# Performance work log

Measured on AMD Instinct MI355X. Metric: run time of the kernel, lower is better.

Reference implementation:

```python
import jax, jax.numpy as jnp
import numpy as np

B, T, C, SIZE = 2, 4096, 1024, 1024
ROPE_DIM = 64
GAMMA = 0.96


def setup_inputs() -> dict:
    key = jax.random.key(0)
    ks = jax.random.split(key, 8)
    x = jax.random.normal(ks[0], (B, T, C), dtype=jnp.float32)
    group_mask = jax.random.randint(ks[1], (B, T), 0, 2).astype(jnp.float32)
    att_mask = jnp.ones((B, T), dtype=jnp.float32)
    # torch init: randn(in, out) / in
    W_Q = jax.random.normal(ks[2], (C, SIZE), dtype=jnp.float32) / C
    W_K = jax.random.normal(ks[3], (C, SIZE), dtype=jnp.float32) / C
    W_V = jax.random.normal(ks[4], (C, SIZE), dtype=jnp.float32) / C
    fc_w = jax.random.normal(ks[5], (SIZE, SIZE), dtype=jnp.float32) / np.float32(np.sqrt(SIZE))
    fc_b = jnp.zeros((SIZE,), dtype=jnp.float32)
    return dict(x=x, group_mask=group_mask, att_mask=att_mask,
                W_Q=W_Q, W_K=W_K, W_V=W_V, fc_w=fc_w, fc_b=fc_b)


def _rope(t, offset):
    # lucidrains rotate_queries_or_keys: rotate first ROPE_DIM features of
    # the last dim, interleaved-pair rotation, positions along axis -2.
    seq = t.shape[-2]
    inv = 1.0 / (10000.0 ** (jnp.arange(0, ROPE_DIM, 2, dtype=jnp.float32) / ROPE_DIM))
    pos = jnp.arange(seq, dtype=jnp.float32) + offset
    freqs = pos[:, None] * inv[None, :]              # [T, D/2]
    freqs = jnp.repeat(freqs, 2, axis=-1)            # [T, D]
    cos, sin = jnp.cos(freqs), jnp.sin(freqs)
    t_rot, t_pass = t[..., :ROPE_DIM], t[..., ROPE_DIM:]
    x1, x2 = t_rot[..., 0::2], t_rot[..., 1::2]
    rot_half = jnp.stack([-x2, x1], axis=-1).reshape(t_rot.shape)
    t_rot = t_rot * cos + rot_half * sin
    return jnp.concatenate([t_rot, t_pass], axis=-1)


def reference(x, group_mask, att_mask, W_Q, W_K, W_V, fc_w, fc_b):
    Bx, Tx, _ = x.shape
    # _qkv with apply_rope=True, apply_act=True (ReLU)
    Q = jax.nn.relu(_rope(x @ W_Q, 0))               # [B,T,SIZE]
    K = jax.nn.relu(_rope(x @ W_K, 0))
    V = jax.nn.relu(x @ W_V)
    n = jnp.arange(Tx)[:, None]
    m = jnp.arange(Tx)[None, :]
    causal = (n >= m)
    # decay mask D[n,m] = gamma^(n-m) for n>=m else 0
    D = jnp.where(causal, jnp.float32(GAMMA) ** (n - m).astype(jnp.float32), 0.0)
    # group mask G[b,n,m] = group_mask[b, n-m] for n>=m else 0
    idx = jnp.clip(n - m, 0, Tx - 1)                 # [T,T]
    G = group_mask[:, idx] * causal.astype(x.dtype)  # [B,T,T]
    A = jnp.einsum('bnd,bmd->bnm', Q, K)
    A = A * att_mask[:, :, None]                     # attention mask
    A = A * D[None, :, :]                            # decay mask
    A = A * G                                        # group mask
    y = jnp.einsum('bnm,bmd->bnd', A, V)
    y = y @ fc_w + fc_b
    return y
```

## Files before the change

kernel.cpp:

```cpp
#include <hip/hip_runtime.h>
#include <stdint.h>

typedef __attribute__((ext_vector_type(4))) float f32x4;
typedef __attribute__((ext_vector_type(8))) __bf16 bf16x8;
typedef __attribute__((ext_vector_type(4))) unsigned short u16x4;
typedef __attribute__((ext_vector_type(8))) unsigned short u16x8;

#define DEV __device__ __forceinline__

DEV unsigned short f2bf(float f) {
  union { float f; unsigned int u; } v; v.f = f;
  unsigned int r = v.u + 0x7fffu + ((v.u >> 16) & 1u);
  return (unsigned short)(r >> 16);
}

DEV void gl_lds16(const void* g, void* l) {
  __builtin_amdgcn_global_load_lds(
      (const __attribute__((address_space(1))) unsigned int*)g,
      (__attribute__((address_space(3))) unsigned int*)l, 16, 0, 0);
}


__global__ void prep_rope(float* __restrict__ costab, float* __restrict__ sintab) {
  int idx = blockIdx.x * 256 + threadIdx.x;
  int n = idx >> 6, c = idx & 63, j = c >> 1;
  float inv = powf(10000.0f, -(float)(2 * j) / 64.0f);
  float ang = (float)n * inv;
  costab[idx] = cosf(ang);
  sintab[idx] = sinf(ang);
}

__global__ void prep_wtab(const float* __restrict__ gm, float* __restrict__ wtab) {
  int t = threadIdx.x;
  int b = t >> 9, d = t & 511;
  wtab[t] = gm[b * 4096 + d] * powf(0.96f, (float)d);
}

__global__ void cvt_x(const float* __restrict__ x, unsigned short* __restrict__ xb) {
  size_t i8 = ((size_t)blockIdx.x * 256 + threadIdx.x) * 8;
  float4 a = *(const float4*)(x + i8);
  float4 b = *(const float4*)(x + i8 + 4);
  u16x8 o;
  o[0] = f2bf(a.x); o[1] = f2bf(a.y); o[2] = f2bf(a.z); o[3] = f2bf(a.w);
  o[4] = f2bf(b.x); o[5] = f2bf(b.y); o[6] = f2bf(b.z); o[7] = f2bf(b.w);
  *(u16x8*)(xb + i8) = o;
}

__global__ void transpose_cvt(const float* __restrict__ src, unsigned short* __restrict__ dst) {
  __shared__ float tile[32][33];
  int tx = threadIdx.x & 31, ty = threadIdx.x >> 5;
  int c0 = blockIdx.x * 32, r0 = blockIdx.y * 32;
  #pragma unroll
  for (int j = 0; j < 4; j++)
    tile[ty + 8 * j][tx] = src[(size_t)(r0 + ty + 8 * j) * 1024 + c0 + tx];
  __syncthreads();
  #pragma unroll
  for (int j = 0; j < 4; j++)
    dst[(size_t)(c0 + ty + 8 * j) * 1024 + r0 + tx] = f2bf(tile[tx][ty + 8 * j]);
}

template<int EPI>
__global__ void __launch_bounds__(256, 2)
gemm128(const unsigned short* __restrict__ A,
        const unsigned short* __restrict__ Bt,
        unsigned short* __restrict__ q_out,
        unsigned short* __restrict__ k_out,
        unsigned short* __restrict__ vt_out,
        const float* __restrict__ costab,
        const float* __restrict__ sintab,
        float* __restrict__ f_out,
        const float* __restrict__ bias)
{
  constexpr int K = 1024;
  __shared__ char smem[32768];
  char* a_sm = smem;
  char* b_sm = smem + 16384;
  const int tid = threadIdx.x;
  const int lane = tid & 63;
  const int w = tid >> 6;
  const int wm = w >> 1, wn = w & 1;
  const int bm = blockIdx.x, bn = blockIdx.y;

  const f32x4 fz = {0.f, 0.f, 0.f, 0.f};
  f32x4 acc[4][4];
  #pragma unroll
  for (int i = 0; i < 4; i++)
    #pragma unroll
    for (int j = 0; j < 4; j++) acc[i][j] = fz;

  const unsigned short* Abase = A + (size_t)bm * 128 * K;
  const unsigned short* Bbase = Bt + (size_t)bn * 128 * K;

  for (int k0 = 0; k0 < K; k0 += 64) {
    __syncthreads();
    #pragma unroll
    for (int i = 0; i < 4; i++) {
      int tg = i * 256 + tid;
      int row = tg >> 3;
      int sl = (tg & 7) ^ (row & 7);
      gl_lds16(Abase + (size_t)row * K + k0 + sl * 8, a_sm + tg * 16);
    }
    #pragma unroll
    for (int i = 0; i < 4; i++) {
      int tg = i * 256 + tid;
      int row = tg >> 3;
      int sl = (tg & 7) ^ (row & 7);
      gl_lds16(Bbase + (size_t)row * K + k0 + sl * 8, b_sm + tg * 16);
    }
    __syncthreads();
    #pragma unroll
    for (int ks = 0; ks < 2; ks++) {
      int kb = ks * 64 + ((lane >> 4) << 4);
      bf16x8 af[4], bfv[4];
      #pragma unroll
      for (int f = 0; f < 4; f++) {
        int ar = wm * 64 + f * 16 + (lane & 15);
        af[f] = *(const bf16x8*)(a_sm + ar * 128 + (kb ^ ((ar & 7) << 4)));
        int br = wn * 64 + f * 16 + (lane & 15);
        bfv[f] = *(const bf16x8*)(b_sm + br * 128 + (kb ^ ((br & 7) << 4)));
      }
      #pragma unroll
      for (int fm = 0; fm < 4; fm++)
        #pragma unroll
        for (int fn = 0; fn < 4; fn++)
          acc[fm][fn] = __builtin_amdgcn_mfma_f32_16x16x32_bf16(af[fm], bfv[fn], acc[fm][fn], 0, 0, 0);
    }
  }

  const int rbase = bm * 128 + wm * 64 + ((lane >> 4) << 2);
  const int cbase = bn * 128 + wn * 64;

  if constexpr (EPI == 0) {
    #pragma unroll
    for (int fn = 0; fn < 4; fn++) {
      int col = cbase + fn * 16 + (lane & 15);
      int which = col >> 10;
      int c = col & 1023;
      #pragma unroll
      for (int fm = 0; fm < 4; fm++) {
        int row0 = rbase + fm * 16;
        float vals[4];
        #pragma unroll
        for (int r = 0; r < 4; r++) vals[r] = acc[fm][fn][r];
        if (which < 2) {
          if (c < 64) {
            #pragma unroll
            for (int r = 0; r < 4; r++) {
              float p = __shfl_xor(vals[r], 1);
              int n = (row0 + r) & 4095;
              float cs = costab[n * 64 + c];
              float sn = sintab[n * 64 + c];
              float rh = (c & 1) ? p : -p;
              vals[r] = vals[r] * cs + rh * sn;
            }
          }
          unsigned short* dst = (which == 0) ? q_out : k_out;
          #pragma unroll
          for (int r = 0; r < 4; r++) {
            float v = vals[r] > 0.f ? vals[r] : 0.f;
            dst[(size_t)(row0 + r) * 1024 + c] = f2bf(v);
          }
        } else {
          u16x4 sv;
          #pragma unroll
          for (int r = 0; r < 4; r++) {
            float v = vals[r] > 0.f ? vals[r] : 0.f;
            sv[r] = f2bf(v);
          }
          *(u16x4*)(vt_out + (size_t)c * 8192 + row0) = sv;
        }
      }
    }
  } else {
    #pragma unroll
    for (int fn = 0; fn < 4; fn++) {
      int col = cbase + fn * 16 + (lane & 15);
      float bv = bias[col];
      #pragma unroll
      for (int fm = 0; fm < 4; fm++) {
        int row0 = rbase + fm * 16;
        #pragma unroll
        for (int r = 0; r < 4; r++)
          f_out[(size_t)(row0 + r) * 1024 + col] = acc[fm][fn][r] + bv;
      }
    }
  }
}

__global__ void __launch_bounds__(512, 2)
attn_kernel(const unsigned short* __restrict__ Qb,
            const unsigned short* __restrict__ Kb,
            const unsigned short* __restrict__ Vt,
            const float* __restrict__ wtab,
            const float* __restrict__ att_mask,
            unsigned short* __restrict__ Yb)
{
  __shared__ char smem[49152];
  __shared__ float wl[320];
  char* k_sm = smem;
  char* q_sm = smem + 40960;
  char* p_sm = smem;

  const int tid = threadIdx.x;
  const int lane = tid & 63;
  const int w = tid >> 6;
  const int q0 = blockIdx.x * 64;
  const int b = blockIdx.y;
  const int base = b * 4096;
  const int kv0 = q0 - 256;

  if (tid < 320) wl[tid] = wtab[b * 512 + tid];

  const int wq = w >> 2, wk = w & 3;
  const f32x4 fz = {0.f, 0.f, 0.f, 0.f};
  f32x4 sacc[2][5];
  #pragma unroll
  for (int i = 0; i < 2; i++)
    #pragma unroll
    for (int j = 0; j < 5; j++) sacc[i][j] = fz;

  for (int c0 = 0; c0 < 1024; c0 += 64) {
    __syncthreads();
    {
      int row = tid >> 3;
      int sl = (tid & 7) ^ (row & 7);
      gl_lds16(Qb + (size_t)(base + q0 + row) * 1024 + c0 + sl * 8, q_sm + tid * 16);
    }
    #pragma unroll
    for (int i = 0; i < 5; i++) {
      int tg = i * 512 + tid;
      int row = tg >> 3;
      int sl = (tg & 7) ^ (row & 7);
      int m = kv0 + row; m = m < 0 ? 0 : m;
      gl_lds16(Kb + (size_t)(base + m) * 1024 + c0 + sl * 8, k_sm + tg * 16);
    }
    __syncthreads();
    #pragma unroll
    for (int ks = 0; ks < 2; ks++) {
      int kb = ks * 64 + ((lane >> 4) << 4);
      bf16x8 af[2], bfv[5];
      #pragma unroll
      for (int f = 0; f < 2; f++) {
        int ar = wq * 32 + f * 16 + (lane & 15);
        af[f] = *(const bf16x8*)(q_sm + ar * 128 + (kb ^ ((ar & 7) << 4)));
      }
      #pragma unroll
      for (int f = 0; f < 5; f++) {
        int br = wk * 80 + f * 16 + (lane & 15);
        bfv[f] = *(const bf16x8*)(k_sm + br * 128 + (kb ^ ((br & 7) << 4)));
      }
      #pragma unroll
      for (int fm = 0; fm < 2; fm++)
        #pragma unroll
        for (int fj = 0; fj < 5; fj++)
          sacc[fm][fj] = __builtin_amdgcn_mfma_f32_16x16x32_bf16(af[fm], bfv[fj], sacc[fm][fj], 0, 0, 0);
    }
  }
  __syncthreads();

  #pragma unroll
  for (int fm = 0; fm < 2; fm++) {
    #pragma unroll
    for (int fj = 0; fj < 5; fj++) {
      int jj = wk * 80 + fj * 16 + (lane & 15);
      int m = kv0 + jj;
      #pragma unroll
      for (int r = 0; r < 4; r++) {
        int i = wq * 32 + fm * 16 + ((lane >> 4) << 2) + r;
        int d = 256 + i - jj;
        float wgt = (d >= 0 && m >= 0) ? wl[d] : 0.f;
        *(unsigned short*)(p_sm + i * 640 + ((jj * 2) ^ ((i & 7) << 4))) =
            f2bf(sacc[fm][fj][r] * wgt);
      }
    }
  }
  __syncthreads();

  f32x4 yacc[4][8];
  #pragma unroll
  for (int i = 0; i < 4; i++)
    #pragma unroll
    for (int j = 0; j < 8; j++) yacc[i][j] = fz;

  for (int kt = 0; kt < 10; kt++) {
    int kb = kt * 64 + ((lane >> 4) << 4);
    bf16x8 pa[4], vb[8];
    #pragma unroll
    for (int f = 0; f < 4; f++) {
      int i = f * 16 + (lane & 15);
      pa[f] = *(const bf16x8*)(p_sm + i * 640 + (kb ^ ((i & 7) << 4)));
    }
    int kvi = kt * 32 + ((lane >> 4) << 3);
    int m = kv0 + kvi; m = m < 0 ? 0 : m;
    #pragma unroll
    for (int f = 0; f < 8; f++) {
      int col = w * 128 + f * 16 + (lane & 15);
      vb[f] = *(const bf16x8*)(Vt + (size_t)col * 8192 + base + m);
    }
    #pragma unroll
    for (int fm = 0; fm < 4; fm++)
      #pragma unroll
      for (int fn = 0; fn < 8; fn++)
        yacc[fm][fn] = __builtin_amdgcn_mfma_f32_16x16x32_bf16(pa[fm], vb[fn], yacc[fm][fn], 0, 0, 0);
  }

  #pragma unroll
  for (int fm = 0; fm < 4; fm++) {
    #pragma unroll
    for (int r = 0; r < 4; r++) {
      int n = q0 + fm * 16 + ((lane >> 4) << 2) + r;
      float am = att_mask[base + n];
      #pragma unroll
      for (int fn = 0; fn < 8; fn++) {
        int col = w * 128 + fn * 16 + (lane & 15);
        Yb[(size_t)(base + n) * 1024 + col] = f2bf(yacc[fm][fn][r] * am);
      }
    }
  }
}

extern "C" void kernel_launch(void* const* d_in, const int* in_sizes, int n_in,
                              void* d_out, int out_size, void* d_ws, size_t ws_size,
                              hipStream_t stream)
{
  (void)in_sizes; (void)n_in; (void)out_size;
  const float* x   = (const float*)d_in[0];
  const float* gm  = (const float*)d_in[1];
  const float* am  = (const float*)d_in[2];
  const float* wq  = (const float*)d_in[3];
  const float* wk  = (const float*)d_in[4];
  const float* wv  = (const float*)d_in[5];
  const float* fcw = (const float*)d_in[6];
  const float* fcb = (const float*)d_in[7];
  float* out = (float*)d_out;

  char* p = (char*)d_ws;
  unsigned short* xb    = (unsigned short*)p; p += (size_t)8192 * 1024 * 2;
  unsigned short* Qb    = (unsigned short*)p; p += (size_t)8192 * 1024 * 2;
  unsigned short* Kb    = (unsigned short*)p; p += (size_t)8192 * 1024 * 2;
  unsigned short* Vt    = (unsigned short*)p; p += (size_t)8192 * 1024 * 2;
  unsigned short* Ybuf  = (unsigned short*)p; p += (size_t)8192 * 1024 * 2;
  unsigned short* WqkvT = (unsigned short*)p; p += (size_t)3072 * 1024 * 2;
  unsigned short* FcwT  = (unsigned short*)p; p += (size_t)1024 * 1024 * 2;
  float* costab = (float*)p; p += (size_t)4096 * 64 * 4;
  float* sintab = (float*)p; p += (size_t)4096 * 64 * 4;
  float* wtab   = (float*)p; p += 4096;
  if ((size_t)(p - (char*)d_ws) > ws_size) return;

  prep_rope<<<1024, 256, 0, stream>>>(costab, sintab);
  prep_wtab<<<1, 1024, 0, stream>>>(gm, wtab);
  cvt_x<<<4096, 256, 0, stream>>>(x, xb);
  transpose_cvt<<<dim3(32, 32), 256, 0, stream>>>(wq, WqkvT);
  transpose_cvt<<<dim3(32, 32), 256, 0, stream>>>(wk, WqkvT + (size_t)1024 * 1024);
  transpose_cvt<<<dim3(32, 32), 256, 0, stream>>>(wv, WqkvT + (size_t)2048 * 1024);
  transpose_cvt<<<dim3(32, 32), 256, 0, stream>>>(fcw, FcwT);

  gemm128<0><<<dim3(64, 24), 256, 0, stream>>>(xb, WqkvT, Qb, Kb, Vt, costab, sintab, nullptr, nullptr);
  attn_kernel<<<dim3(64, 2), 512, 0, stream>>>(Qb, Kb, Vt, wtab, am, Ybuf);
  gemm128<1><<<dim3(64, 8), 256, 0, stream>>>(Ybuf, FcwT, nullptr, nullptr, nullptr, nullptr, nullptr, out, fcb);
}
```

Baseline: 244.9 us.

## Replace QKV GEMM with 256x256 pipelined tile kernel and merge prep launches

Adds a new QKV projection GEMM that uses 256x256 tiles with 512 threads and 128KB of dynamic LDS. It double-buffers half-tiles with direct global-to-LDS loads, uses explicit waitcnt, barriers and setprio to overlap loads with MFMA work, and keeps the RoPE/ReLU epilogue. The goal is higher data reuse per tile and better overlap of memory and compute. The rope and wtab prep kernels are merged into one launch, and the four weight transposes into one 3D-grid launch, to cut launch count. The trade-offs are a large LDS footprint that limits occupancy, and hand-tuned wait counts that are fragile.

```diff
diff --git a/kernel.cpp b/kernel.cpp
--- a/kernel.cpp
+++ b/kernel.cpp
@@ -20,20 +20,25 @@
       (__attribute__((address_space(3))) unsigned int*)l, 16, 0, 0);
 }
 
-
-__global__ void prep_rope(float* __restrict__ costab, float* __restrict__ sintab) {
+#define SBAR() __builtin_amdgcn_s_barrier()
+#define LGKM0() do { asm volatile("s_waitcnt lgkmcnt(0)" ::: "memory"); __builtin_amdgcn_sched_barrier(0); } while (0)
+#define VMC6() do { asm volatile("s_waitcnt vmcnt(6)" ::: "memory"); __builtin_amdgcn_sched_barrier(0); } while (0)
+#define VMC0() do { asm volatile("s_waitcnt vmcnt(0)" ::: "memory"); __builtin_amdgcn_sched_barrier(0); } while (0)
+
+
+__global__ void prep_tabs(const float* __restrict__ gm,
+                          float* __restrict__ costab, float* __restrict__ sintab,
+                          float* __restrict__ wtab) {
   int idx = blockIdx.x * 256 + threadIdx.x;
   int n = idx >> 6, c = idx & 63, j = c >> 1;
   float inv = powf(10000.0f, -(float)(2 * j) / 64.0f);
   float ang = (float)n * inv;
   costab[idx] = cosf(ang);
   sintab[idx] = sinf(ang);
-}
-
-__global__ void prep_wtab(const float* __restrict__ gm, float* __restrict__ wtab) {
-  int t = threadIdx.x;
-  int b = t >> 9, d = t & 511;
-  wtab[t] = gm[b * 4096 + d] * powf(0.96f, (float)d);
+  if (idx < 1024) {
+    int b = idx >> 9, d = idx & 511;
+    wtab[idx] = gm[b * 4096 + d] * powf(0.96f, (float)d);
+  }
 }
 
 __global__ void cvt_x(const float* __restrict__ x, unsigned short* __restrict__ xb) {
@@ -46,8 +51,13 @@
   *(u16x8*)(xb + i8) = o;
 }
 
-__global__ void transpose_cvt(const float* __restrict__ src, unsigned short* __restrict__ dst) {
+__global__ void transpose_cvt4(const float* __restrict__ s0, const float* __restrict__ s1,
+                               const float* __restrict__ s2, const float* __restrict__ s3,
+                               unsigned short* __restrict__ d0, unsigned short* __restrict__ d3) {
   __shared__ float tile[32][33];
+  int z = blockIdx.z;
+  const float* src = (z == 0) ? s0 : (z == 1) ? s1 : (z == 2) ? s2 : s3;
+  unsigned short* dst = (z == 3) ? d3 : d0 + (size_t)z * 1024 * 1024;
   int tx = threadIdx.x & 31, ty = threadIdx.x >> 5;
   int c0 = blockIdx.x * 32, r0 = blockIdx.y * 32;
   #pragma unroll
@@ -59,17 +69,189 @@
     dst[(size_t)(c0 + ty + 8 * j) * 1024 + r0 + tx] = f2bf(tile[tx][ty + 8 * j]);
 }
 
-template<int EPI>
+
+DEV void stage_half(const unsigned short* __restrict__ g0, int kcol, char* regn, int tid) {
+  #pragma unroll
+  for (int i = 0; i < 2; i++) {
+    int tg = i * 512 + tid;
+    int row = tg >> 3;
+    int ch = tg & 7;
+    gl_lds16(g0 + (size_t)row * 1024 + kcol + ((ch ^ (row & 7)) << 3), regn + tg * 16);
+  }
+}
+
+DEV void read_a4(bf16x8 (&af)[4][2], const char* regn, int wm, int lane) {
+  #pragma unroll
+  for (int f = 0; f < 4; f++) {
+    int row = wm * 64 + f * 16 + (lane & 15);
+    #pragma unroll
+    for (int ks = 0; ks < 2; ks++) {
+      int c = ks * 4 + (lane >> 4);
+      af[f][ks] = *(const bf16x8*)(regn + row * 128 + ((c ^ (row & 7)) << 4));
+    }
+  }
+}
+
+DEV void read_b2(bf16x8 (&bfr)[2][2], const char* regn, int wn, int lane) {
+  #pragma unroll
+  for (int g = 0; g < 2; g++) {
+    int row = wn * 32 + g * 16 + (lane & 15);
+    #pragma unroll
+    for (int ks = 0; ks < 2; ks++) {
+      int c = ks * 4 + (lane >> 4);
+      bfr[g][ks] = *(const bf16x8*)(regn + row * 128 + ((c ^ (row & 7)) << 4));
+    }
+  }
+}
+
+template<int MB, int NB>
+DEV void mfma16(f32x4 (&acc)[8][4], const bf16x8 (&af)[4][2], const bf16x8 (&bfr)[2][2]) {
+  #pragma unroll
+  for (int ks = 0; ks < 2; ks++)
+    #pragma unroll
+    for (int f = 0; f < 4; f++)
+      #pragma unroll
+      for (int g = 0; g < 2; g++)
+        acc[MB + f][NB + g] =
+            __builtin_amdgcn_mfma_f32_16x16x32_bf16(af[f][ks], bfr[g][ks], acc[MB + f][NB + g], 0, 0, 0);
+}
+
+__global__ void __launch_bounds__(512, 2)
+gemm256_qkv(const unsigned short* __restrict__ A,
+            const unsigned short* __restrict__ Bt,
+            unsigned short* __restrict__ q_out,
+            unsigned short* __restrict__ k_out,
+            unsigned short* __restrict__ vt_out,
+            const float* __restrict__ costab,
+            const float* __restrict__ sintab)
+{
+  extern __shared__ char smem[];
+  constexpr int K = 1024, NT = 16;
+  const int tid = threadIdx.x;
+  const int lane = tid & 63;
+  const int w = tid >> 6;
+  const int wm = w >> 2, wn = w & 3;
+  const int bm = blockIdx.x, bn = blockIdx.y;
+
+  char* rg[2][2][2];
+  #pragma unroll
+  for (int d = 0; d < 2; d++)
+    #pragma unroll
+    for (int m = 0; m < 2; m++)
+      #pragma unroll
+      for (int h = 0; h < 2; h++)
+        rg[d][m][h] = smem + d * 65536 + m * 32768 + h * 16384;
+
+  const unsigned short* Ab = A + (size_t)bm * 256 * K;
+  const unsigned short* Bb = Bt + (size_t)bn * 256 * K;
+  const unsigned short* A0g = Ab;
+  const unsigned short* A1g = Ab + (size_t)128 * K;
+  const unsigned short* B0g = Bb;
+  const unsigned short* B1g = Bb + (size_t)128 * K;
+
+  const f32x4 fz = {0.f, 0.f, 0.f, 0.f};
+  f32x4 acc[8][4];
+  #pragma unroll
+  for (int i = 0; i < 8; i++)
+    #pragma unroll
+    for (int j = 0; j < 4; j++) acc[i][j] = fz;
+
+  stage_half(A0g, 0, rg[0][0][0], tid);
+  stage_half(B0g, 0, rg[0][1][0], tid);
+  stage_half(B1g, 0, rg[0][1][1], tid);
+  stage_half(A1g, 0, rg[0][0][1], tid);
+  stage_half(A0g, 64, rg[1][0][0], tid);
+  stage_half(B1g, 64, rg[1][1][1], tid);
+  stage_half(A1g, 64, rg[1][0][1], tid);
+  VMC6();
+  SBAR();
+
+  for (int t = 0; t < NT; ++t) {
+    const int db = t & 1;
+    bf16x8 af[4][2], bfr[2][2];
+
+    read_a4(af, rg[db][0][0], wm, lane);
+    read_b2(bfr, rg[db][1][0], wn, lane);
+    if (t + 1 < NT) stage_half(B0g, (t + 1) * 64, rg[db ^ 1][1][0], tid);
+    SBAR(); LGKM0();
+    __builtin_amdgcn_s_setprio(1);
+    mfma16<0, 0>(acc, af, bfr);
+    __builtin_amdgcn_s_setprio(0);
+    SBAR();
+
+    read_b2(bfr, rg[db][1][1], wn, lane);
+    if (t + 2 < NT) stage_half(A0g, (t + 2) * 64, rg[db][0][0], tid);
+    SBAR(); LGKM0();
+    __builtin_amdgcn_s_setprio(1);
+    mfma16<0, 2>(acc, af, bfr);
+    __builtin_amdgcn_s_setprio(0);
+    SBAR();
+
+    read_a4(af, rg[db][0][1], wm, lane);
+    if (t + 2 < NT) stage_half(B1g, (t + 2) * 64, rg[db][1][1], tid);
+    SBAR(); LGKM0();
+    __builtin_amdgcn_s_setprio(1);
+    mfma16<4, 2>(acc, af, bfr);
+    __builtin_amdgcn_s_setprio(0);
+    SBAR();
+
+    read_b2(bfr, rg[db][1][0], wn, lane);
+    if (t + 2 < NT) stage_half(A1g, (t + 2) * 64, rg[db][0][1], tid);
+    SBAR(); LGKM0();
+    __builtin_amdgcn_s_setprio(1);
+    mfma16<4, 0>(acc, af, bfr);
+    __builtin_amdgcn_s_setprio(0);
+    if (t < NT - 2) { VMC6(); } else { VMC0(); }
+    SBAR();
+  }
+
+  #pragma unroll
+  for (int n = 0; n < 4; n++) {
+    int col = bn * 256 + (n >> 1) * 128 + wn * 32 + (n & 1) * 16 + (lane & 15);
+    int which = col >> 10;
+    int c = col & 1023;
+    #pragma unroll
+    for (int m = 0; m < 8; m++) {
+      int row0 = bm * 256 + (m >> 2) * 128 + wm * 64 + (m & 3) * 16 + ((lane >> 4) << 2);
+      float vals[4];
+      #pragma unroll
+      for (int r = 0; r < 4; r++) vals[r] = acc[m][n][r];
+      if (which < 2) {
+        if (c < 64) {
+          #pragma unroll
+          for (int r = 0; r < 4; r++) {
+            float p = __shfl_xor(vals[r], 1);
+            int nn = (row0 + r) & 4095;
+            float cs = costab[nn * 64 + c];
+            float sn = sintab[nn * 64 + c];
+            float rh = (c & 1) ? p : -p;
+            vals[r] = vals[r] * cs + rh * sn;
+          }
+        }
+        unsigned short* dst = (which == 0) ? q_out : k_out;
+        #pragma unroll
+        for (int r = 0; r < 4; r++) {
+          float v = vals[r] > 0.f ? vals[r] : 0.f;
+          dst[(size_t)(row0 + r) * 1024 + c] = f2bf(v);
+        }
+      } else {
+        u16x4 sv;
+        #pragma unroll
+        for (int r = 0; r < 4; r++) {
+          float v = vals[r] > 0.f ? vals[r] : 0.f;
+          sv[r] = f2bf(v);
+        }
+        *(u16x4*)(vt_out + (size_t)c * 8192 + row0) = sv;
+      }
+    }
+  }
+}
+
 __global__ void __launch_bounds__(256, 2)
-gemm128(const unsigned short* __restrict__ A,
-        const unsigned short* __restrict__ Bt,
-        unsigned short* __restrict__ q_out,
-        unsigned short* __restrict__ k_out,
-        unsigned short* __restrict__ vt_out,
-        const float* __restrict__ costab,
-        const float* __restrict__ sintab,
-        float* __restrict__ f_out,
-        const float* __restrict__ bias)
+gemm128_fc(const unsigned short* __restrict__ A,
+           const unsigned short* __restrict__ Bt,
+           float* __restrict__ f_out,
+           const float* __restrict__ bias)
 {
   constexpr int K = 1024;
   __shared__ char smem[32768];
@@ -129,60 +311,16 @@
 
   const int rbase = bm * 128 + wm * 64 + ((lane >> 4) << 2);
   const int cbase = bn * 128 + wn * 64;
-
-  if constexpr (EPI == 0) {
-    #pragma unroll
-    for (int fn = 0; fn < 4; fn++) {
-      int col = cbase + fn * 16 + (lane & 15);
-      int which = col >> 10;
-      int c = col & 1023;
-      #pragma unroll
-      for (int fm = 0; fm < 4; fm++) {
-        int row0 = rbase + fm * 16;
-        float vals[4];
-        #pragma unroll
-        for (int r = 0; r < 4; r++) vals[r] = acc[fm][fn][r];
-        if (which < 2) {
-          if (c < 64) {
-            #pragma unroll
-            for (int r = 0; r < 4; r++) {
-              float p = __shfl_xor(vals[r], 1);
-              int n = (row0 + r) & 4095;
-              float cs = costab[n * 64 + c];
-              float sn = sintab[n * 64 + c];
-              float rh = (c & 1) ? p : -p;
-              vals[r] = vals[r] * cs + rh * sn;
-            }
-          }
-          unsigned short* dst = (which == 0) ? q_out : k_out;
-          #pragma unroll
-          for (int r = 0; r < 4; r++) {
-            float v = vals[r] > 0.f ? vals[r] : 0.f;
-            dst[(size_t)(row0 + r) * 1024 + c] = f2bf(v);
-          }
-        } else {
-          u16x4 sv;
-          #pragma unroll
-          for (int r = 0; r < 4; r++) {
-            float v = vals[r] > 0.f ? vals[r] : 0.f;
-            sv[r] = f2bf(v);
-          }
-          *(u16x4*)(vt_out + (size_t)c * 8192 + row0) = sv;
-        }
-      }
-    }
-  } else {
-    #pragma unroll
-    for (int fn = 0; fn < 4; fn++) {
-      int col = cbase + fn * 16 + (lane & 15);
-      float bv = bias[col];
-      #pragma unroll
-      for (int fm = 0; fm < 4; fm++) {
-        int row0 = rbase + fm * 16;
-        #pragma unroll
-        for (int r = 0; r < 4; r++)
-          f_out[(size_t)(row0 + r) * 1024 + col] = acc[fm][fn][r] + bv;
-      }
+  #pragma unroll
+  for (int fn = 0; fn < 4; fn++) {
+    int col = cbase + fn * 16 + (lane & 15);
+    float bv = bias[col];
+    #pragma unroll
+    for (int fm = 0; fm < 4; fm++) {
+      int row0 = rbase + fm * 16;
+      #pragma unroll
+      for (int r = 0; r < 4; r++)
+        f_out[(size_t)(row0 + r) * 1024 + col] = acc[fm][fn][r] + bv;
     }
   }
 }
@@ -347,15 +485,14 @@
   float* wtab   = (float*)p; p += 4096;
   if ((size_t)(p - (char*)d_ws) > ws_size) return;
 
-  prep_rope<<<1024, 256, 0, stream>>>(costab, sintab);
-  prep_wtab<<<1, 1024, 0, stream>>>(gm, wtab);
+  hipFuncSetAttribute((const void*)gemm256_qkv,
+                      hipFuncAttributeMaxDynamicSharedMemorySize, 131072);
+
+  prep_tabs<<<1024, 256, 0, stream>>>(gm, costab, sintab, wtab);
   cvt_x<<<4096, 256, 0, stream>>>(x, xb);
-  transpose_cvt<<<dim3(32, 32), 256, 0, stream>>>(wq, WqkvT);
-  transpose_cvt<<<dim3(32, 32), 256, 0, stream>>>(wk, WqkvT + (size_t)1024 * 1024);
-  transpose_cvt<<<dim3(32, 32), 256, 0, stream>>>(wv, WqkvT + (size_t)2048 * 1024);
-  transpose_cvt<<<dim3(32, 32), 256, 0, stream>>>(fcw, FcwT);
-
-  gemm128<0><<<dim3(64, 24), 256, 0, stream>>>(xb, WqkvT, Qb, Kb, Vt, costab, sintab, nullptr, nullptr);
+  transpose_cvt4<<<dim3(32, 32, 4), 256, 0, stream>>>(wq, wk, wv, fcw, WqkvT, FcwT);
+
+  gemm256_qkv<<<dim3(32, 12), 512, 131072, stream>>>(xb, WqkvT, Qb, Kb, Vt, costab, sintab);
   attn_kernel<<<dim3(64, 2), 512, 0, stream>>>(Qb, Kb, Vt, wtab, am, Ybuf);
-  gemm128<1><<<dim3(64, 8), 256, 0, stream>>>(Ybuf, FcwT, nullptr, nullptr, nullptr, nullptr, nullptr, out, fcb);
-}
+  gemm128_fc<<<dim3(64, 8), 256, 0, stream>>>(Ybuf, FcwT, out, fcb);
+}
```

Measured after the change: 308.1 us. +25.8%, slower.
